# Optimization experiments

Measured on AMD Instinct MI355X. Metric: run time of the kernel, lower is better.

The kernel has to match this reference:

```python
import jax, jax.numpy as jnp
import numpy as np

DIM = 512
HID = 1024
E = 8          # num_experts
K = 2          # num_experts_per_tok
B, S = 4, 2048


def setup_inputs() -> dict:
    key = jax.random.key(0)
    ks = jax.random.split(key, 10)
    sd = DIM ** -0.5
    sh = HID ** -0.5
    return {
        "x": jax.random.normal(ks[0], (B, S, DIM), dtype=jnp.float32),
        "gate_w": jax.random.normal(ks[1], (E, DIM), dtype=jnp.float32) * sd,
        "biases": jnp.zeros((E,), dtype=jnp.float32),  # e_expert_biases
        # routed experts: swiglu  y = (silu(x@w1) * (x@w3)) @ w2
        "w1": jax.random.normal(ks[2], (E, DIM, HID), dtype=jnp.float32) * sd,
        "w3": jax.random.normal(ks[3], (E, DIM, HID), dtype=jnp.float32) * sd,
        "w2": jax.random.normal(ks[4], (E, HID, DIM), dtype=jnp.float32) * sh,
        # single shared expert
        "sw1": jax.random.normal(ks[5], (DIM, HID), dtype=jnp.float32) * sd,
        "sw3": jax.random.normal(ks[6], (DIM, HID), dtype=jnp.float32) * sd,
        "sw2": jax.random.normal(ks[7], (HID, DIM), dtype=jnp.float32) * sh,
    }


def reference(x, gate_w, biases, w1, w3, w2, sw1, sw3, sw2):
    Bb, Ss, D = x.shape
    xt = x.reshape(Bb * Ss, D)                      # [T, D]

    # shared expert (applied to full x)
    shared = (jax.nn.silu(xt @ sw1) * (xt @ sw3)) @ sw2  # [T, D]

    # router
    scores = xt @ gate_w.T                          # [T, E]
    # indices chosen from biased scores (aux-free load balancing)
    _, idx = jax.lax.top_k(scores + biases, K)      # [T, K] int
    # gate values are top-k of the UNBIASED scores (as in original code)
    topv, _ = jax.lax.top_k(scores, K)              # [T, K]
    p = jax.nn.sigmoid(topv)
    p = p / jnp.sum(p, axis=-1, keepdims=True)      # [T, K]

    # every expert on every token (dense-combine MoE reference)
    h = jax.nn.silu(jnp.einsum('td,edh->eth', xt, w1)) * jnp.einsum('td,edh->eth', xt, w3)
    y = jnp.einsum('eth,ehd->etd', h, w2)           # [E, T, D]

    onehot = jax.nn.one_hot(idx, E, dtype=xt.dtype)  # [T, K, E]
    comb = jnp.einsum('tk,tke->te', p, onehot)       # [T, E] combine weights
    out = jnp.einsum('te,etd->td', comb, y) + shared
    return out.reshape(Bb, Ss, D)
```

## Files before the change

### kernel.cpp

```cpp
#include <hip/hip_runtime.h>
#include <hip/hip_bf16.h>


#define Tn 8192
#define Dd 512
#define Hh 1024
#define NEx 9

typedef __attribute__((ext_vector_type(8))) short short8;
typedef __attribute__((ext_vector_type(4))) float f32x4;

#define AS1 __attribute__((address_space(1)))
#define AS3 __attribute__((address_space(3)))

#define OFF_XB    ((size_t)0)
#define OFF_W13T  (OFF_XB + (size_t)Tn * Dd * 2)
#define OFF_W2T   (OFF_W13T + (size_t)NEx * 2 * Hh * Dd * 2)
#define OFF_HBUF  (OFF_W2T + (size_t)NEx * Dd * Hh * 2)
#define OFF_TOK   (OFF_HBUF + (size_t)(3 * Tn) * Hh * 2)
#define OFF_SLOTP (OFF_TOK + (size_t)8 * Tn * 4)
#define OFF_PG    (OFF_SLOTP + (size_t)Tn * 2 * 4)
#define OFF_CNT   (OFF_PG + (size_t)Tn * 2 * 4)
#define OFF_OFFS  (OFF_CNT + 1024)
#define OFF_YC    OFF_XB

__device__ __forceinline__ ushort f2bf(float f) {
    unsigned int u = __float_as_uint(f);
    return (ushort)((u + 0x7fffu + ((u >> 16) & 1u)) >> 16);
}
__device__ __forceinline__ float bf2f(short s) {
    return __uint_as_float(((unsigned int)(unsigned short)s) << 16);
}

__global__ __launch_bounds__(256) void trans_kernel(
        const float* __restrict__ w1, const float* __restrict__ sw1,
        const float* __restrict__ w3, const float* __restrict__ sw3,
        const float* __restrict__ w2, const float* __restrict__ sw2,
        ushort* __restrict__ w13t, ushort* __restrict__ w2t) {
    __shared__ float tile[32][33];
    int z = blockIdx.z;
    int fam = z / 9, sl = z - fam * 9;
    int tx = threadIdx.x & 31, ty = threadIdx.x >> 5;
    if (fam < 2) {
        const float* base = (fam == 0) ? ((sl < 8) ? w1 + (size_t)sl * Dd * Hh : sw1)
                                       : ((sl < 8) ? w3 + (size_t)sl * Dd * Hh : sw3);
        ushort* dst = w13t + (size_t)sl * 2 * Hh * Dd;
        int c0 = blockIdx.x * 32, r0 = blockIdx.y * 32;
#pragma unroll
        for (int k = 0; k < 4; ++k)
            tile[ty + 8 * k][tx] = base[(size_t)(r0 + ty + 8 * k) * Hh + c0 + tx];
        __syncthreads();
#pragma unroll
        for (int k = 0; k < 4; ++k) {
            int h = c0 + ty + 8 * k;
            int n = (((h >> 4) * 2 + fam) << 4) + (h & 15);
            dst[(size_t)n * Dd + r0 + tx] = f2bf(tile[tx][ty + 8 * k]);
        }
    } else {
        const float* base = (sl < 8) ? w2 + (size_t)sl * Dd * Hh : sw2;
        ushort* dst = w2t + (size_t)sl * Dd * Hh;
        int r0 = blockIdx.x * 32, c0 = blockIdx.y * 32;
#pragma unroll
        for (int k = 0; k < 4; ++k)
            tile[ty + 8 * k][tx] = base[(size_t)(r0 + ty + 8 * k) * Dd + c0 + tx];
        __syncthreads();
#pragma unroll
        for (int k = 0; k < 4; ++k)
            dst[(size_t)(c0 + ty + 8 * k) * Hh + r0 + tx] = f2bf(tile[tx][ty + 8 * k]);
    }
}

__global__ __launch_bounds__(256) void router_kernel(const float* __restrict__ x,
                                                     const float* __restrict__ gw,
                                                     const float* __restrict__ bias,
                                                     int* __restrict__ cnt,
                                                     int* __restrict__ tok,
                                                     int* __restrict__ slotp,
                                                     float* __restrict__ pg,
                                                     ushort* __restrict__ xb) {
    __shared__ int le[64];
    __shared__ float lg[64];
    __shared__ int lpos[64];
    __shared__ int lcnt[8];
    __shared__ int gbase[8];
    int tid = threadIdx.x, lane = tid & 63, wave = tid >> 6;
    if (tid < 8) lcnt[tid] = 0;
    __syncthreads();
    int t0 = blockIdx.x * 32 + wave * 8;
    for (int it = 0; it < 8; ++it) {
        int t = t0 + it;
        const float4* xr = (const float4*)(x + (size_t)t * Dd);
        float4 xa = xr[lane * 2], xc = xr[lane * 2 + 1];
        ushort4 o1, o2;
        o1.x = f2bf(xa.x); o1.y = f2bf(xa.y); o1.z = f2bf(xa.z); o1.w = f2bf(xa.w);
        o2.x = f2bf(xc.x); o2.y = f2bf(xc.y); o2.z = f2bf(xc.z); o2.w = f2bf(xc.w);
        *(ushort4*)(xb + (size_t)t * Dd + lane * 8) = o1;
        *(ushort4*)(xb + (size_t)t * Dd + lane * 8 + 4) = o2;
        float sc[8];
#pragma unroll
        for (int e = 0; e < 8; ++e) {
            const float4* gr = (const float4*)(gw + (size_t)e * Dd);
            float4 ga = gr[lane * 2], gc = gr[lane * 2 + 1];
            float s = xa.x * ga.x + xa.y * ga.y + xa.z * ga.z + xa.w * ga.w
                    + xc.x * gc.x + xc.y * gc.y + xc.z * gc.z + xc.w * gc.w;
#pragma unroll
            for (int o = 32; o > 0; o >>= 1) s += __shfl_xor(s, o);
            sc[e] = s;
        }
        if (lane == 0) {
            float b0 = -1e30f; int i0 = 0;
#pragma unroll
            for (int e = 0; e < 8; ++e) { float bv = sc[e] + bias[e]; if (bv > b0) { b0 = bv; i0 = e; } }
            float b1v = -1e30f; int i1 = (i0 == 0) ? 1 : 0;
#pragma unroll
            for (int e = 0; e < 8; ++e) if (e != i0) { float bv = sc[e] + bias[e]; if (bv > b1v) { b1v = bv; i1 = e; } }
            float v0 = -1e30f; int k0i = 0;
#pragma unroll
            for (int e = 0; e < 8; ++e) if (sc[e] > v0) { v0 = sc[e]; k0i = e; }
            float v1 = -1e30f;
#pragma unroll
            for (int e = 0; e < 8; ++e) if (e != k0i && sc[e] > v1) v1 = sc[e];
            float p0 = 1.f / (1.f + __expf(-v0));
            float p1 = 1.f / (1.f + __expf(-v1));
            float inv = 1.f / (p0 + p1);
            int ai = (wave * 8 + it) * 2;
            le[ai] = i0;     lg[ai] = p0 * inv;
            le[ai + 1] = i1; lg[ai + 1] = p1 * inv;
        }
    }
    __syncthreads();
    if (tid < 64) lpos[tid] = atomicAdd(&lcnt[le[tid]], 1);
    __syncthreads();
    if (tid < 8) gbase[tid] = atomicAdd(&cnt[tid * 32], lcnt[tid]);
    __syncthreads();
    if (tid < 64) {
        int e = le[tid];
        int dst = gbase[e] + lpos[tid];
        int t = blockIdx.x * 32 + (tid >> 1);
        tok[(size_t)e * Tn + dst] = t;
        slotp[t * 2 + (tid & 1)] = (e << 16) | dst;
        pg[t * 2 + (tid & 1)] = lg[tid];
    }
}

__global__ void scan_kernel(const int* cnt, int* off, int* cntc) {
    if (threadIdx.x == 0 && blockIdx.x == 0) {
        int s = 0;
        for (int e = 0; e < 8; ++e) { int c = cnt[e * 32]; cntc[e] = c; off[e] = s; s += c; }
        off[8] = s;
        cntc[8] = Tn;
    }
}

__global__ __launch_bounds__(256, 2) void stage1_kernel(
        const ushort* __restrict__ xb, const ushort* __restrict__ w13t,
        const int* __restrict__ tok, const int* __restrict__ cntc,
        const int* __restrict__ off, ushort* __restrict__ Hbuf) {
    int b = blockIdx.x;
    int xcd = b & 7, slot = b >> 3;
    int e, xblk, yblk;
    if (slot < 1024) { e = xcd; xblk = slot >> 4; yblk = slot & 15; }
    else { int s = slot - 1024; e = 8; xblk = (xcd << 3) + (s >> 4); yblk = s & 15; }
    int cn = cntc[e];
    int m0 = xblk * 128;
    if (m0 >= cn) return;
    int n0 = yblk * 128;
    const ushort* we = w13t + (size_t)e * 2 * Hh * Dd;

    __shared__ ushort As[128 * 64];
    __shared__ ushort Bs[128 * 64];
    __shared__ int toks[128];

    int tid = threadIdx.x;
    if (tid < 128) {
        int sl2 = m0 + tid;
        int sl = sl2 < cn ? sl2 : cn - 1;
        toks[tid] = (e == 8) ? sl : tok[(size_t)e * Tn + sl];
    }
    __syncthreads();

    int lane = tid & 63, wave = tid >> 6;
    int wm = (wave & 1) * 64, wn = (wave >> 1) * 64;
    int col15 = lane & 15, quad = lane >> 4;
    int lr = lane >> 3;
    int lcx = ((lane & 7) ^ lr) * 8;

    f32x4 acc[4][4];
#pragma unroll
    for (int a = 0; a < 4; ++a)
#pragma unroll
        for (int b2 = 0; b2 < 4; ++b2) acc[a][b2] = (f32x4){0.f, 0.f, 0.f, 0.f};

    for (int kb = 0; kb < Dd; kb += 64) {
#pragma unroll
        for (int i = 0; i < 4; ++i) {
            int cid = wave * 4 + i;
            const ushort* g = xb + (size_t)toks[cid * 8 + lr] * Dd + kb + lcx;
            __builtin_amdgcn_global_load_lds((const AS1 void*)g, (AS3 void*)(As + cid * 512), 16, 0, 0);
        }
#pragma unroll
        for (int i = 0; i < 4; ++i) {
            int cid = wave * 4 + i;
            const ushort* g = we + (size_t)(n0 + cid * 8 + lr) * Dd + kb + lcx;
            __builtin_amdgcn_global_load_lds((const AS1 void*)g, (AS3 void*)(Bs + cid * 512), 16, 0, 0);
        }
        __syncthreads();
#pragma unroll
        for (int ks = 0; ks < 2; ++ks) {
            int px = ((ks * 4 + quad) ^ (col15 & 7)) * 8;
            short8 a[4], b2[4];
#pragma unroll
            for (int mi = 0; mi < 4; ++mi)
                a[mi] = *(const short8*)&As[(wm + mi * 16 + col15) * 64 + px];
#pragma unroll
            for (int ni = 0; ni < 4; ++ni)
                b2[ni] = *(const short8*)&Bs[(wn + ni * 16 + col15) * 64 + px];
#pragma unroll
            for (int mi = 0; mi < 4; ++mi)
#pragma unroll
                for (int ni = 0; ni < 4; ++ni)
                    acc[mi][ni] = __builtin_amdgcn_mfma_f32_16x16x32_bf16(a[mi], b2[ni], acc[mi][ni], 0, 0, 0);
        }
        __syncthreads();
    }

    int oe = off[e];
    int hbase = (n0 + wn) >> 1;
#pragma unroll
    for (int mi = 0; mi < 4; ++mi)
#pragma unroll
        for (int r = 0; r < 4; ++r) {
            int sl2 = m0 + wm + mi * 16 + quad * 4 + r;
            if (sl2 < cn) {
                size_t rowb = (size_t)(oe + sl2) * Hh;
#pragma unroll
                for (int np = 0; np < 2; ++np) {
                    float h1 = acc[mi][np * 2][r], h3 = acc[mi][np * 2 + 1][r];
                    float s = h1 / (1.f + __expf(-h1));
                    Hbuf[rowb + hbase + np * 16 + col15] = f2bf(s * h3);
                }
            }
        }
}

__global__ __launch_bounds__(256, 3) void stage2_kernel(
        const ushort* __restrict__ Hbuf, const ushort* __restrict__ w2t,
        const int* __restrict__ cntc, const int* __restrict__ off,
        ushort* __restrict__ Yc) {
    int b = blockIdx.x;
    int xcd = b & 7, slot = b >> 3;
    int e, xblk, yblk;
    if (slot < 256) { e = xcd; xblk = slot >> 2; yblk = slot & 3; }
    else { int s = slot - 256; e = 8; xblk = (xcd << 3) + (s >> 2); yblk = s & 3; }
    int cn = cntc[e];
    int m0 = xblk * 128;
    if (m0 >= cn) return;
    int n0 = yblk * 128;
    int oe = off[e];
    const ushort* w2e = w2t + (size_t)e * Dd * Hh;

    __shared__ ushort As[128 * 64];
    __shared__ ushort Bs[128 * 64];

    int tid = threadIdx.x;
    int lane = tid & 63, wave = tid >> 6;
    int wm = (wave & 1) * 64, wn = (wave >> 1) * 64;
    int col15 = lane & 15, quad = lane >> 4;
    int lr = lane >> 3;
    int lcx = ((lane & 7) ^ lr) * 8;

    f32x4 acc[4][4];
#pragma unroll
    for (int a = 0; a < 4; ++a)
#pragma unroll
        for (int b2 = 0; b2 < 4; ++b2) acc[a][b2] = (f32x4){0.f, 0.f, 0.f, 0.f};

    for (int kb = 0; kb < Hh; kb += 64) {
#pragma unroll
        for (int i = 0; i < 4; ++i) {
            int cid = wave * 4 + i;
            const ushort* g = Hbuf + (size_t)(oe + m0 + cid * 8 + lr) * Hh + kb + lcx;
            __builtin_amdgcn_global_load_lds((const AS1 void*)g, (AS3 void*)(As + cid * 512), 16, 0, 0);
        }
#pragma unroll
        for (int i = 0; i < 4; ++i) {
            int cid = wave * 4 + i;
            const ushort* g = w2e + (size_t)(n0 + cid * 8 + lr) * Hh + kb + lcx;
            __builtin_amdgcn_global_load_lds((const AS1 void*)g, (AS3 void*)(Bs + cid * 512), 16, 0, 0);
        }
        __syncthreads();
#pragma unroll
        for (int ks = 0; ks < 2; ++ks) {
            int px = ((ks * 4 + quad) ^ (col15 & 7)) * 8;
            short8 a[4], b2[4];
#pragma unroll
            for (int mi = 0; mi < 4; ++mi)
                a[mi] = *(const short8*)&As[(wm + mi * 16 + col15) * 64 + px];
#pragma unroll
            for (int ni = 0; ni < 4; ++ni)
                b2[ni] = *(const short8*)&Bs[(wn + ni * 16 + col15) * 64 + px];
#pragma unroll
            for (int mi = 0; mi < 4; ++mi)
#pragma unroll
                for (int ni = 0; ni < 4; ++ni)
                    acc[mi][ni] = __builtin_amdgcn_mfma_f32_16x16x32_bf16(a[mi], b2[ni], acc[mi][ni], 0, 0, 0);
        }
        __syncthreads();
    }

#pragma unroll
    for (int mi = 0; mi < 4; ++mi)
#pragma unroll
        for (int r = 0; r < 4; ++r) {
            int sl2 = m0 + wm + mi * 16 + quad * 4 + r;
            if (sl2 < cn) {
                size_t rowb = (size_t)(oe + sl2) * Dd;
#pragma unroll
                for (int ni = 0; ni < 4; ++ni)
                    Yc[rowb + n0 + wn + ni * 16 + col15] = f2bf(acc[mi][ni][r]);
            }
        }
}

__global__ __launch_bounds__(256) void combine_kernel(const ushort* __restrict__ Yc,
        const int* __restrict__ slotp, const float* __restrict__ pg,
        const int* __restrict__ off, float* __restrict__ out) {
    int g = blockIdx.x * 256 + threadIdx.x;
    int t = g >> 6;
    int c = (g & 63) * 8;
    int p0 = slotp[t * 2], p1 = slotp[t * 2 + 1];
    float g0 = pg[t * 2], g1 = pg[t * 2 + 1];
    int s0 = off[p0 >> 16] + (p0 & 0xffff);
    int s1 = off[p1 >> 16] + (p1 & 0xffff);
    int s2 = off[8] + t;
    short8 a = *(const short8*)(Yc + (size_t)s0 * Dd + c);
    short8 b = *(const short8*)(Yc + (size_t)s1 * Dd + c);
    short8 d = *(const short8*)(Yc + (size_t)s2 * Dd + c);
    float o[8];
#pragma unroll
    for (int i = 0; i < 8; ++i)
        o[i] = g0 * bf2f(a[i]) + g1 * bf2f(b[i]) + bf2f(d[i]);
    float* dst = out + (size_t)t * Dd + c;
    *(float4*)dst = (float4){o[0], o[1], o[2], o[3]};
    *(float4*)(dst + 4) = (float4){o[4], o[5], o[6], o[7]};
}

extern "C" void kernel_launch(void* const* d_in, const int* in_sizes, int n_in,
                              void* d_out, int out_size, void* d_ws, size_t ws_size,
                              hipStream_t stream) {
    (void)in_sizes; (void)n_in; (void)out_size; (void)ws_size;
    const float* x    = (const float*)d_in[0];
    const float* gw   = (const float*)d_in[1];
    const float* bias = (const float*)d_in[2];
    const float* w1   = (const float*)d_in[3];
    const float* w3   = (const float*)d_in[4];
    const float* w2   = (const float*)d_in[5];
    const float* sw1  = (const float*)d_in[6];
    const float* sw3  = (const float*)d_in[7];
    const float* sw2  = (const float*)d_in[8];
    float* out = (float*)d_out;

    char* ws = (char*)d_ws;
    ushort* xb    = (ushort*)(ws + OFF_XB);
    ushort* w13t  = (ushort*)(ws + OFF_W13T);
    ushort* w2t   = (ushort*)(ws + OFF_W2T);
    ushort* Hbuf  = (ushort*)(ws + OFF_HBUF);
    ushort* Yc    = (ushort*)(ws + OFF_YC);
    int*    tok   = (int*)(ws + OFF_TOK);
    int*    slotp = (int*)(ws + OFF_SLOTP);
    float*  pg    = (float*)(ws + OFF_PG);
    int*    cnt   = (int*)(ws + OFF_CNT);
    int*    off   = (int*)(ws + OFF_OFFS);
    int*    cntc  = off + 16;

    hipMemsetAsync(cnt, 0, 1024, stream);

    trans_kernel<<<dim3(32, 16, 27), 256, 0, stream>>>(w1, sw1, w3, sw3, w2, sw2, w13t, w2t);
    router_kernel<<<256, 256, 0, stream>>>(x, gw, bias, cnt, tok, slotp, pg, xb);
    scan_kernel<<<1, 64, 0, stream>>>(cnt, off, cntc);

    stage1_kernel<<<9216, 256, 0, stream>>>(xb, w13t, tok, cntc, off, Hbuf);
    stage2_kernel<<<2304, 256, 0, stream>>>(Hbuf, w2t, cntc, off, Yc);
    combine_kernel<<<2048, 256, 0, stream>>>(Yc, slotp, pg, off, out);
}
```

Measured before the change: 240.1 us.

## Fuse transpose, router and scan into one preprocessing kernel; hoist GEMM load addresses

Merges the weight transpose/convert kernel, the router kernel and the single-thread scan kernel into one launch. Blocks 0-255 do routing and blocks 256 onward do the transposes. The last router block, found with an atomic counter and a threadfence, computes the expert offsets. This removes two kernel launches and their serialization gaps. It also precomputes the per-thread global load pointers in both GEMM stages and fully unrolls the k-loop, which trims address arithmetic but may raise register pressure.

```diff
diff --git a/kernel.cpp b/kernel.cpp
--- a/kernel.cpp
+++ b/kernel.cpp
@@ -32,61 +32,65 @@
     return __uint_as_float(((unsigned int)(unsigned short)s) << 16);
 }
 
-__global__ __launch_bounds__(256) void trans_kernel(
+__global__ __launch_bounds__(256) void preproc_kernel(
+        const float* __restrict__ x, const float* __restrict__ gw,
+        const float* __restrict__ bias,
         const float* __restrict__ w1, const float* __restrict__ sw1,
         const float* __restrict__ w3, const float* __restrict__ sw3,
         const float* __restrict__ w2, const float* __restrict__ sw2,
-        ushort* __restrict__ w13t, ushort* __restrict__ w2t) {
+        ushort* __restrict__ w13t, ushort* __restrict__ w2t,
+        int* __restrict__ cnt, int* __restrict__ tok,
+        int* __restrict__ slotp, float* __restrict__ pg,
+        ushort* __restrict__ xb, int* __restrict__ off, int* __restrict__ cntc) {
     __shared__ float tile[32][33];
-    int z = blockIdx.z;
-    int fam = z / 9, sl = z - fam * 9;
-    int tx = threadIdx.x & 31, ty = threadIdx.x >> 5;
-    if (fam < 2) {
-        const float* base = (fam == 0) ? ((sl < 8) ? w1 + (size_t)sl * Dd * Hh : sw1)
-                                       : ((sl < 8) ? w3 + (size_t)sl * Dd * Hh : sw3);
-        ushort* dst = w13t + (size_t)sl * 2 * Hh * Dd;
-        int c0 = blockIdx.x * 32, r0 = blockIdx.y * 32;
-#pragma unroll
-        for (int k = 0; k < 4; ++k)
-            tile[ty + 8 * k][tx] = base[(size_t)(r0 + ty + 8 * k) * Hh + c0 + tx];
-        __syncthreads();
-#pragma unroll
-        for (int k = 0; k < 4; ++k) {
-            int h = c0 + ty + 8 * k;
-            int n = (((h >> 4) * 2 + fam) << 4) + (h & 15);
-            dst[(size_t)n * Dd + r0 + tx] = f2bf(tile[tx][ty + 8 * k]);
-        }
-    } else {
-        const float* base = (sl < 8) ? w2 + (size_t)sl * Dd * Hh : sw2;
-        ushort* dst = w2t + (size_t)sl * Dd * Hh;
-        int r0 = blockIdx.x * 32, c0 = blockIdx.y * 32;
-#pragma unroll
-        for (int k = 0; k < 4; ++k)
-            tile[ty + 8 * k][tx] = base[(size_t)(r0 + ty + 8 * k) * Dd + c0 + tx];
-        __syncthreads();
-#pragma unroll
-        for (int k = 0; k < 4; ++k)
-            dst[(size_t)(c0 + ty + 8 * k) * Hh + r0 + tx] = f2bf(tile[tx][ty + 8 * k]);
-    }
-}
-
-__global__ __launch_bounds__(256) void router_kernel(const float* __restrict__ x,
-                                                     const float* __restrict__ gw,
-                                                     const float* __restrict__ bias,
-                                                     int* __restrict__ cnt,
-                                                     int* __restrict__ tok,
-                                                     int* __restrict__ slotp,
-                                                     float* __restrict__ pg,
-                                                     ushort* __restrict__ xb) {
     __shared__ int le[64];
     __shared__ float lg[64];
     __shared__ int lpos[64];
     __shared__ int lcnt[8];
     __shared__ int gbase[8];
-    int tid = threadIdx.x, lane = tid & 63, wave = tid >> 6;
+    int bb = blockIdx.x;
+    int tid = threadIdx.x;
+
+    if (bb >= 256) {
+        int tb = bb - 256;
+        int z = tb >> 9;
+        int fam = z / 9, sl = z - fam * 9;
+        int bxx = tb & 31, byy = (tb >> 5) & 15;
+        int tx = tid & 31, ty = tid >> 5;
+        if (fam < 2) {
+            const float* base = (fam == 0) ? ((sl < 8) ? w1 + (size_t)sl * Dd * Hh : sw1)
+                                           : ((sl < 8) ? w3 + (size_t)sl * Dd * Hh : sw3);
+            ushort* dst = w13t + (size_t)sl * 2 * Hh * Dd;
+            int c0 = bxx * 32, r0 = byy * 32;
+#pragma unroll
+            for (int k = 0; k < 4; ++k)
+                tile[ty + 8 * k][tx] = base[(size_t)(r0 + ty + 8 * k) * Hh + c0 + tx];
+            __syncthreads();
+#pragma unroll
+            for (int k = 0; k < 4; ++k) {
+                int h = c0 + ty + 8 * k;
+                int n = (((h >> 4) * 2 + fam) << 4) + (h & 15);
+                dst[(size_t)n * Dd + r0 + tx] = f2bf(tile[tx][ty + 8 * k]);
+            }
+        } else {
+            const float* base = (sl < 8) ? w2 + (size_t)sl * Dd * Hh : sw2;
+            ushort* dst = w2t + (size_t)sl * Dd * Hh;
+            int r0 = bxx * 32, c0 = byy * 32;
+#pragma unroll
+            for (int k = 0; k < 4; ++k)
+                tile[ty + 8 * k][tx] = base[(size_t)(r0 + ty + 8 * k) * Dd + c0 + tx];
+            __syncthreads();
+#pragma unroll
+            for (int k = 0; k < 4; ++k)
+                dst[(size_t)(c0 + ty + 8 * k) * Hh + r0 + tx] = f2bf(tile[tx][ty + 8 * k]);
+        }
+        return;
+    }
+
+    int lane = tid & 63, wave = tid >> 6;
     if (tid < 8) lcnt[tid] = 0;
     __syncthreads();
-    int t0 = blockIdx.x * 32 + wave * 8;
+    int t0 = bb * 32 + wave * 8;
     for (int it = 0; it < 8; ++it) {
         int t = t0 + it;
         const float4* xr = (const float4*)(x + (size_t)t * Dd);
@@ -136,19 +140,23 @@
     if (tid < 64) {
         int e = le[tid];
         int dst = gbase[e] + lpos[tid];
-        int t = blockIdx.x * 32 + (tid >> 1);
+        int t = bb * 32 + (tid >> 1);
         tok[(size_t)e * Tn + dst] = t;
         slotp[t * 2 + (tid & 1)] = (e << 16) | dst;
         pg[t * 2 + (tid & 1)] = lg[tid];
     }
-}
-
-__global__ void scan_kernel(const int* cnt, int* off, int* cntc) {
-    if (threadIdx.x == 0 && blockIdx.x == 0) {
-        int s = 0;
-        for (int e = 0; e < 8; ++e) { int c = cnt[e * 32]; cntc[e] = c; off[e] = s; s += c; }
-        off[8] = s;
-        cntc[8] = Tn;
+    __syncthreads();
+    if (tid == 0) {
+        __threadfence();
+        if (atomicAdd(&cnt[16], 1) == 255) {
+            int s = 0;
+            for (int e = 0; e < 8; ++e) {
+                int c = atomicAdd(&cnt[e * 32], 0);
+                cntc[e] = c; off[e] = s; s += c;
+            }
+            off[8] = s;
+            cntc[8] = Tn;
+        }
     }
 }
 
@@ -185,25 +193,29 @@
     int lr = lane >> 3;
     int lcx = ((lane & 7) ^ lr) * 8;
 
+    const ushort* gA[4];
+    const ushort* gB[4];
+#pragma unroll
+    for (int i = 0; i < 4; ++i) {
+        int cid = wave * 4 + i;
+        gA[i] = xb + (size_t)toks[cid * 8 + lr] * Dd + lcx;
+        gB[i] = we + (size_t)(n0 + cid * 8 + lr) * Dd + lcx;
+    }
+
     f32x4 acc[4][4];
 #pragma unroll
     for (int a = 0; a < 4; ++a)
 #pragma unroll
         for (int b2 = 0; b2 < 4; ++b2) acc[a][b2] = (f32x4){0.f, 0.f, 0.f, 0.f};
 
+#pragma unroll
     for (int kb = 0; kb < Dd; kb += 64) {
 #pragma unroll
-        for (int i = 0; i < 4; ++i) {
-            int cid = wave * 4 + i;
-            const ushort* g = xb + (size_t)toks[cid * 8 + lr] * Dd + kb + lcx;
-            __builtin_amdgcn_global_load_lds((const AS1 void*)g, (AS3 void*)(As + cid * 512), 16, 0, 0);
-        }
-#pragma unroll
-        for (int i = 0; i < 4; ++i) {
-            int cid = wave * 4 + i;
-            const ushort* g = we + (size_t)(n0 + cid * 8 + lr) * Dd + kb + lcx;
-            __builtin_amdgcn_global_load_lds((const AS1 void*)g, (AS3 void*)(Bs + cid * 512), 16, 0, 0);
-        }
+        for (int i = 0; i < 4; ++i)
+            __builtin_amdgcn_global_load_lds((const AS1 void*)(gA[i] + kb), (AS3 void*)(As + (wave * 4 + i) * 512), 16, 0, 0);
+#pragma unroll
+        for (int i = 0; i < 4; ++i)
+            __builtin_amdgcn_global_load_lds((const AS1 void*)(gB[i] + kb), (AS3 void*)(Bs + (wave * 4 + i) * 512), 16, 0, 0);
         __syncthreads();
 #pragma unroll
         for (int ks = 0; ks < 2; ++ks) {
@@ -269,25 +281,29 @@
     int lr = lane >> 3;
     int lcx = ((lane & 7) ^ lr) * 8;
 
+    const ushort* gA[4];
+    const ushort* gB[4];
+#pragma unroll
+    for (int i = 0; i < 4; ++i) {
+        int cid = wave * 4 + i;
+        gA[i] = Hbuf + (size_t)(oe + m0 + cid * 8 + lr) * Hh + lcx;
+        gB[i] = w2e + (size_t)(n0 + cid * 8 + lr) * Hh + lcx;
+    }
+
     f32x4 acc[4][4];
 #pragma unroll
     for (int a = 0; a < 4; ++a)
 #pragma unroll
         for (int b2 = 0; b2 < 4; ++b2) acc[a][b2] = (f32x4){0.f, 0.f, 0.f, 0.f};
 
+#pragma unroll
     for (int kb = 0; kb < Hh; kb += 64) {
 #pragma unroll
-        for (int i = 0; i < 4; ++i) {
-            int cid = wave * 4 + i;
-            const ushort* g = Hbuf + (size_t)(oe + m0 + cid * 8 + lr) * Hh + kb + lcx;
-            __builtin_amdgcn_global_load_lds((const AS1 void*)g, (AS3 void*)(As + cid * 512), 16, 0, 0);
-        }
-#pragma unroll
-        for (int i = 0; i < 4; ++i) {
-            int cid = wave * 4 + i;
-            const ushort* g = w2e + (size_t)(n0 + cid * 8 + lr) * Hh + kb + lcx;
-            __builtin_amdgcn_global_load_lds((const AS1 void*)g, (AS3 void*)(Bs + cid * 512), 16, 0, 0);
-        }
+        for (int i = 0; i < 4; ++i)
+            __builtin_amdgcn_global_load_lds((const AS1 void*)(gA[i] + kb), (AS3 void*)(As + (wave * 4 + i) * 512), 16, 0, 0);
+#pragma unroll
+        for (int i = 0; i < 4; ++i)
+            __builtin_amdgcn_global_load_lds((const AS1 void*)(gB[i] + kb), (AS3 void*)(Bs + (wave * 4 + i) * 512), 16, 0, 0);
         __syncthreads();
 #pragma unroll
         for (int ks = 0; ks < 2; ++ks) {
@@ -375,10 +391,8 @@
 
     hipMemsetAsync(cnt, 0, 1024, stream);
 
-    trans_kernel<<<dim3(32, 16, 27), 256, 0, stream>>>(w1, sw1, w3, sw3, w2, sw2, w13t, w2t);
-    router_kernel<<<256, 256, 0, stream>>>(x, gw, bias, cnt, tok, slotp, pg, xb);
-    scan_kernel<<<1, 64, 0, stream>>>(cnt, off, cntc);
-
+    preproc_kernel<<<14080, 256, 0, stream>>>(x, gw, bias, w1, sw1, w3, sw3, w2, sw2,
+                                              w13t, w2t, cnt, tok, slotp, pg, xb, off, cntc);
     stage1_kernel<<<9216, 256, 0, stream>>>(xb, w13t, tok, cntc, off, Hbuf);
     stage2_kernel<<<2304, 256, 0, stream>>>(Hbuf, w2t, cntc, off, Yc);
     combine_kernel<<<2048, 256, 0, stream>>>(Yc, slotp, pg, off, out);
```

Result: no change. 239.9 us (-0.1%).
